# Kernel tuning notes

Measured on AMD Instinct MI355X. Metric: run time of the kernel, lower is better.

## Reference

```python
import jax, jax.numpy as jnp
import numpy as np

N_NODES = 100000
N_EDGES = 3200000
IN_DIM = 128
OUT_DIM = 256  # transform outputs OUT_DIM//2, concat -> OUT_DIM


def setup_inputs() -> dict:
    key = jax.random.key(0)
    ks = jax.random.split(key, 8)
    feats = jax.random.normal(ks[0], (N_NODES, IN_DIM), dtype=jnp.float32)
    src = jax.random.randint(ks[1], (N_EDGES,), 0, N_NODES, dtype=jnp.int64)
    dst = jax.random.randint(ks[2], (N_EDGES,), 0, N_NODES, dtype=jnp.int64)
    # KernelMLP(128, 128, n_hidden=2, scale_hidden=2): 128 -> 256 -> 512 -> 128
    def lin(k, fan_in, fan_out):
        s = 1.0 / np.sqrt(fan_in)
        return jax.random.uniform(k, (fan_in, fan_out), jnp.float32, -s, s)
    W1 = lin(ks[3], 128, 256)
    W2 = lin(ks[4], 256, 512)
    W3 = lin(ks[5], 512, 128)
    b1 = jnp.zeros((256,), jnp.float32)
    b2 = jnp.zeros((512,), jnp.float32)
    b3 = jnp.zeros((128,), jnp.float32)
    return {"features": feats, "src": src, "dst": dst,
            "W1": W1, "b1": b1, "W2": W2, "b2": b2, "W3": W3, "b3": b3}


def kernel_mlp(x, W1, b1, W2, b2, W3, b3):
    # per-node MLP with hidden widths scaling by scale_hidden, ReLU between layers
    h = jax.nn.relu(x @ W1 + b1)
    h = jax.nn.relu(h @ W2 + b2)
    return h @ W3 + b3  # [N, out_dim//2]


def reference(features, src, dst, W1, b1, W2, b2, W3, b3):
    h = kernel_mlp(features, W1, b1, W2, b2, W3, b3)  # [N, 64*2]
    # update_all(copy_src, sum): agg[d] = sum_{(s,d) in E} h[s]
    msgs = h[src]  # [E, out_dim//2] gather (memory bound)
    agg = jax.ops.segment_sum(msgs, dst, num_segments=features.shape[0])
    return jnp.concatenate([h, agg], axis=-1)  # [N, out_dim]
```

## Files before the change

kernel.cpp:

```cpp
#include <hip/hip_runtime.h>
#include <hip/hip_bf16.h>
#include <hip/hip_fp16.h>

typedef __attribute__((ext_vector_type(8))) short short8;
typedef __attribute__((ext_vector_type(4))) short short4v;
typedef __attribute__((ext_vector_type(4))) float f32x4;

#define TM 64
#define SX 136
#define S1 264

#define BK_LG 6
#define BK_N  64
#define MAX_NB 4096
#define PS_CHUNK 16384

__device__ __forceinline__ short f2bf(float x) {
    union { float f; unsigned u; } v; v.f = x;
    unsigned r = v.u + 0x7fffu + ((v.u >> 16) & 1u);
    return (short)(r >> 16);
}

__global__ __launch_bounds__(256) void prep_weights(
        const float* __restrict__ W1, const float* __restrict__ W2,
        const float* __restrict__ W3,
        short* __restrict__ W1t, short* __restrict__ W2t, short* __restrict__ W3t) {
    int i = blockIdx.x * 256 + threadIdx.x;
    if (i < 32768) {
        int n = i >> 7, k = i & 127;
        W1t[i] = f2bf(W1[k * 256 + n]);
    } else if (i < 32768 + 131072) {
        int j = i - 32768;
        int n = j >> 8, k = j & 255;
        W2t[j] = f2bf(W2[k * 512 + n]);
    } else if (i < 229376) {
        int j = i - 163840;
        int n = j >> 9, k = j & 511;
        W3t[j] = f2bf(W3[k * 128 + n]);
    }
}

__global__ __launch_bounds__(512) void mlp_kernel(
        const float* __restrict__ X,
        const float* __restrict__ b1f, const float* __restrict__ b2f,
        const float* __restrict__ b3f,
        const short* __restrict__ W1t, const short* __restrict__ W2t,
        const short* __restrict__ W3t,
        float* __restrict__ out, __half* __restrict__ hh, int n_nodes) {
    __shared__ short lds[TM * S1 + TM * SX];
    short* ldsH1 = lds;
    short* ldsX  = lds + TM * S1;
    short* ldsH2 = ldsX;

    const int tid  = threadIdx.x;
    const int ch   = tid >> 6;
    const int lane = tid & 63;
    const int ln   = lane & 15;
    const int quad = lane >> 4;
    const long node0 = (long)blockIdx.x * TM;

    for (int i = tid; i < TM * 32; i += 512) {
        int r = i >> 5, c4 = i & 31;
        long node = node0 + r;
        float4 v = make_float4(0.f, 0.f, 0.f, 0.f);
        if (node < n_nodes) v = *(const float4*)&X[node * 128 + c4 * 4];
        short4v s;
        s.x = f2bf(v.x); s.y = f2bf(v.y); s.z = f2bf(v.z); s.w = f2bf(v.w);
        *(short4v*)&ldsX[r * SX + c4 * 4] = s;
    }
    __syncthreads();

#pragma unroll
    for (int nt = 0; nt < 2; ++nt) {
        int n = ch * 32 + nt * 16 + ln;
        const short* bp = &W1t[n * 128 + quad * 8];
        short8 b[4];
#pragma unroll
        for (int kk = 0; kk < 4; ++kk) b[kk] = *(const short8*)(bp + kk * 32);
        float bias = b1f[n];
#pragma unroll
        for (int m = 0; m < 4; ++m) {
            f32x4 c = {0.f, 0.f, 0.f, 0.f};
#pragma unroll
            for (int kk = 0; kk < 4; ++kk) {
                short8 a = *(const short8*)&ldsX[(m * 16 + ln) * SX + kk * 32 + quad * 8];
                c = __builtin_amdgcn_mfma_f32_16x16x32_bf16(a, b[kk], c, 0, 0, 0);
            }
#pragma unroll
            for (int rr = 0; rr < 4; ++rr) {
                float h = c[rr] + bias;
                h = h > 0.f ? h : 0.f;
                ldsH1[(m * 16 + quad * 4 + rr) * S1 + n] = f2bf(h);
            }
        }
    }
    __syncthreads();

    f32x4 acc3[4] = {};
#pragma unroll 1
    for (int cc = 0; cc < 4; ++cc) {
        {
            int n2 = cc * 128 + ch * 16 + ln;
            const short* bp = &W2t[n2 * 256 + quad * 8];
            short8 b[8];
#pragma unroll
            for (int kk = 0; kk < 8; ++kk) b[kk] = *(const short8*)(bp + kk * 32);
            float bias = b2f[n2];
            int nl = ch * 16 + ln;
#pragma unroll
            for (int m = 0; m < 4; ++m) {
                f32x4 c = {0.f, 0.f, 0.f, 0.f};
#pragma unroll
                for (int kk = 0; kk < 8; ++kk) {
                    short8 a = *(const short8*)&ldsH1[(m * 16 + ln) * S1 + kk * 32 + quad * 8];
                    c = __builtin_amdgcn_mfma_f32_16x16x32_bf16(a, b[kk], c, 0, 0, 0);
                }
#pragma unroll
                for (int rr = 0; rr < 4; ++rr) {
                    float h = c[rr] + bias;
                    h = h > 0.f ? h : 0.f;
                    ldsH2[(m * 16 + quad * 4 + rr) * SX + nl] = f2bf(h);
                }
            }
        }
        __syncthreads();

        {
            int n3 = ch * 16 + ln;
            const short* bp = &W3t[n3 * 512 + cc * 128 + quad * 8];
            short8 b[4];
#pragma unroll
            for (int kk = 0; kk < 4; ++kk) b[kk] = *(const short8*)(bp + kk * 32);
#pragma unroll
            for (int m = 0; m < 4; ++m) {
#pragma unroll
                for (int kk = 0; kk < 4; ++kk) {
                    short8 a = *(const short8*)&ldsH2[(m * 16 + ln) * SX + kk * 32 + quad * 8];
                    acc3[m] = __builtin_amdgcn_mfma_f32_16x16x32_bf16(a, b[kk], acc3[m], 0, 0, 0);
                }
            }
        }
        __syncthreads();
    }

    {
        int n3 = ch * 16 + ln;
        float bias = b3f[n3];
#pragma unroll
        for (int m = 0; m < 4; ++m) {
#pragma unroll
            for (int rr = 0; rr < 4; ++rr) {
                long node = node0 + m * 16 + quad * 4 + rr;
                if (node < n_nodes) {
                    float v = acc3[m][rr] + bias;
                    out[node * 256 + n3] = v;
                    if (hh) hh[node * 128 + n3] = __float2half(v);
                }
            }
        }
    }
}


__global__ __launch_bounds__(256) void bhist_kernel(
        const int* __restrict__ dst, int* __restrict__ bcnt,
        int n_edges, int nb) {
    __shared__ int h[MAX_NB];
    int tid = threadIdx.x;
    for (int b = tid; b < nb; b += 256) h[b] = 0;
    __syncthreads();
    for (int e = blockIdx.x * 256 + tid; e < n_edges; e += gridDim.x * 256)
        atomicAdd(&h[dst[e] >> BK_LG], 1);
    __syncthreads();
    for (int b = tid; b < nb; b += 256) {
        int c = h[b];
        if (c) atomicAdd(&bcnt[b], c);
    }
}

__global__ __launch_bounds__(256) void bscan_kernel(
        const int* __restrict__ bcnt, int* __restrict__ boffs,
        int* __restrict__ bcur, int nb) {
    __shared__ int s[256];
    int t = threadIdx.x;
    int per = (nb + 255) >> 8;
    int lo = t * per;
    int sum = 0;
    for (int i = 0; i < per; ++i) {
        int b = lo + i;
        if (b < nb) sum += bcnt[b];
    }
    s[t] = sum;
    __syncthreads();
#pragma unroll
    for (int off = 1; off < 256; off <<= 1) {
        int v = (t >= off) ? s[t - off] : 0;
        __syncthreads();
        s[t] += v;
        __syncthreads();
    }
    int base = (t == 0) ? 0 : s[t - 1];
    for (int i = 0; i < per; ++i) {
        int b = lo + i;
        if (b < nb) {
            int c = bcnt[b];
            boffs[b] = base;
            bcur[b]  = base;
            base += c;
        }
    }
    if (t == 255) boffs[nb] = s[255];
}

__global__ __launch_bounds__(256) void bscatter_kernel(
        const int* __restrict__ src, const int* __restrict__ dst,
        int* __restrict__ bcur, unsigned* __restrict__ pairs,
        int n_edges, int nb) {
    __shared__ int h[MAX_NB];
    int tid = threadIdx.x;
    long e0 = (long)blockIdx.x * PS_CHUNK;
    int cnt = n_edges - (int)e0;
    if (cnt > PS_CHUNK) cnt = PS_CHUNK;
    if (cnt <= 0) return;
    for (int b = tid; b < nb; b += 256) h[b] = 0;
    __syncthreads();
    for (int i = tid; i < cnt; i += 256)
        atomicAdd(&h[dst[e0 + i] >> BK_LG], 1);
    __syncthreads();
    for (int b = tid; b < nb; b += 256) {
        int c = h[b];
        h[b] = c ? atomicAdd(&bcur[b], c) : 0;
    }
    __syncthreads();
    for (int i = tid; i < cnt; i += 256) {
        int d = dst[e0 + i];
        int s = src[e0 + i];
        int p = atomicAdd(&h[d >> BK_LG], 1);
        pairs[p] = ((unsigned)(d & (BK_N - 1)) << 26) | (unsigned)s;
    }
}

__global__ __launch_bounds__(256) void bsort_kernel(
        const unsigned* __restrict__ pairs, const int* __restrict__ boffs,
        int* __restrict__ offs, int* __restrict__ esrc,
        int n_nodes, int n_edges) {
    __shared__ int hist[BK_N];
    __shared__ int cur[BK_N];
    const int tid = threadIdx.x;
    const int b = blockIdx.x;
    const int base = boffs[b];
    const int cnt = boffs[b + 1] - base;

    if (tid < BK_N) hist[tid] = 0;
    __syncthreads();
    for (int i = tid; i < cnt; i += 256)
        atomicAdd(&hist[pairs[base + i] >> 26], 1);
    __syncthreads();
    if (tid == 0) {
        int run = base;
#pragma unroll
        for (int k = 0; k < BK_N; ++k) { cur[k] = run; run += hist[k]; }
    }
    __syncthreads();
    if (tid < BK_N) {
        int node = (b << BK_LG) + tid;
        if (node < n_nodes) offs[node] = cur[tid];
    }
    if (b == 0 && tid == 0) offs[n_nodes] = n_edges;
    __syncthreads();
    for (int i = tid; i < cnt; i += 256) {
        unsigned p = pairs[base + i];
        int pos = atomicAdd(&cur[p >> 26], 1);
        esrc[pos] = (int)(p & 0x03FFFFFFu);
    }
}

__global__ __launch_bounds__(256) void agg_half_kernel(
        const int* __restrict__ esrc, const int* __restrict__ offs,
        const __half* __restrict__ hh, float* __restrict__ out, int n_nodes) {
    int node = blockIdx.x * 4 + (threadIdx.x >> 6);
    if (node >= n_nodes) return;
    const int l2 = (threadIdx.x & 63) * 2;
    const int s0 = offs[node];
    const int s1 = offs[node + 1];
    float ax = 0.f, ay = 0.f;
    int j = s0;
    for (; j + 8 <= s1; j += 8) {
        int s[8];
#pragma unroll
        for (int u = 0; u < 8; ++u) s[u] = esrc[j + u];
        __half2 v[8];
#pragma unroll
        for (int u = 0; u < 8; ++u) v[u] = *(const __half2*)&hh[(long)s[u] * 128 + l2];
#pragma unroll
        for (int u = 0; u < 8; ++u) {
            float2 f = __half22float2(v[u]);
            ax += f.x; ay += f.y;
        }
    }
    for (; j < s1; ++j) {
        float2 f = __half22float2(*(const __half2*)&hh[(long)esrc[j] * 128 + l2]);
        ax += f.x; ay += f.y;
    }
    *(float2*)&out[(long)node * 256 + 128 + l2] = make_float2(ax, ay);
}

__global__ __launch_bounds__(256) void agg_kernel(
        const int* __restrict__ esrc, const int* __restrict__ offs,
        float* __restrict__ out, int n_nodes) {
    int node = blockIdx.x * 4 + (threadIdx.x >> 6);
    if (node >= n_nodes) return;
    const int l2 = (threadIdx.x & 63) * 2;
    const int s0 = offs[node];
    const int s1 = offs[node + 1];
    float ax = 0.f, ay = 0.f;
    int j = s0;
    for (; j + 8 <= s1; j += 8) {
        int s[8];
#pragma unroll
        for (int u = 0; u < 8; ++u) s[u] = esrc[j + u];
        float2 v[8];
#pragma unroll
        for (int u = 0; u < 8; ++u) v[u] = *(const float2*)&out[(long)s[u] * 256 + l2];
#pragma unroll
        for (int u = 0; u < 8; ++u) { ax += v[u].x; ay += v[u].y; }
    }
    for (; j < s1; ++j) {
        float2 v = *(const float2*)&out[(long)esrc[j] * 256 + l2];
        ax += v.x; ay += v.y;
    }
    *(float2*)&out[(long)node * 256 + 128 + l2] = make_float2(ax, ay);
}

__global__ __launch_bounds__(256) void bagg_kernel(
        const unsigned* __restrict__ pairs, const int* __restrict__ boffs,
        float* __restrict__ out, int n_nodes) {
    __shared__ float acc[BK_N * 128];
    __shared__ unsigned eb[512];
    const int tid  = threadIdx.x;
    const int col  = tid & 127;
    const int half = tid >> 7;
    const int node0 = blockIdx.x << BK_LG;

    for (int i = tid; i < BK_N * 128; i += 256) acc[i] = 0.f;

    const int s0 = boffs[blockIdx.x];
    const int s1 = boffs[blockIdx.x + 1];

    for (int j0 = s0; j0 < s1; j0 += 512) {
        int m = s1 - j0;
        if (m > 512) m = 512;
        for (int i = tid; i < m; i += 256) eb[i] = pairs[j0 + i];
        __syncthreads();
        int i = half;
        for (; i + 8 <= m; i += 8) {
            unsigned p0 = eb[i], p1 = eb[i + 2], p2 = eb[i + 4], p3 = eb[i + 6];
            float v0 = out[(long)(p0 & 0x03FFFFFFu) * 256 + col];
            float v1 = out[(long)(p1 & 0x03FFFFFFu) * 256 + col];
            float v2 = out[(long)(p2 & 0x03FFFFFFu) * 256 + col];
            float v3 = out[(long)(p3 & 0x03FFFFFFu) * 256 + col];
            atomicAdd(&acc[(p0 >> 26) * 128 + col], v0);
            atomicAdd(&acc[(p1 >> 26) * 128 + col], v1);
            atomicAdd(&acc[(p2 >> 26) * 128 + col], v2);
            atomicAdd(&acc[(p3 >> 26) * 128 + col], v3);
        }
        for (; i < m; i += 2) {
            unsigned pk = eb[i];
            float v = out[(long)(pk & 0x03FFFFFFu) * 256 + col];
            atomicAdd(&acc[(pk >> 26) * 128 + col], v);
        }
        __syncthreads();
    }

    for (int i = tid; i < BK_N * 128; i += 256) {
        int n = node0 + (i >> 7);
        if (n < n_nodes) out[(long)n * 256 + 128 + (i & 127)] = acc[i];
    }
}

__global__ __launch_bounds__(256) void zero_agg(float* __restrict__ out, int n_nodes) {
    int i = blockIdx.x * 256 + threadIdx.x;
    int total = n_nodes * 32;
    for (; i < total; i += gridDim.x * 256) {
        int n = i >> 5, q = i & 31;
        *(float4*)&out[(long)n * 256 + 128 + q * 4] = make_float4(0.f, 0.f, 0.f, 0.f);
    }
}

__global__ __launch_bounds__(256) void edge_agg(
        const int* __restrict__ src, const int* __restrict__ dst,
        float* __restrict__ out, int n_edges) {
    int e = blockIdx.x * 8 + (threadIdx.x >> 5);
    if (e >= n_edges) return;
    int l = threadIdx.x & 31;
    long s = src[e];
    long d = dst[e];
    const float4 v = *(const float4*)&out[s * 256 + l * 4];
    float* p = &out[d * 256 + 128 + l * 4];
    unsafeAtomicAdd(p + 0, v.x);
    unsafeAtomicAdd(p + 1, v.y);
    unsafeAtomicAdd(p + 2, v.z);
    unsafeAtomicAdd(p + 3, v.w);
}

extern "C" void kernel_launch(void* const* d_in, const int* in_sizes, int n_in,
                              void* d_out, int out_size, void* d_ws, size_t ws_size,
                              hipStream_t stream) {
    const float* X   = (const float*)d_in[0];
    const int*   src = (const int*)d_in[1];
    const int*   dst = (const int*)d_in[2];
    const float* W1  = (const float*)d_in[3];
    const float* b1  = (const float*)d_in[4];
    const float* W2  = (const float*)d_in[5];
    const float* b2  = (const float*)d_in[6];
    const float* W3  = (const float*)d_in[7];
    const float* b3  = (const float*)d_in[8];
    float* out = (float*)d_out;

    const int n_nodes = in_sizes[0] / 128;
    const int n_edges = in_sizes[1];
    const int nb = (n_nodes + BK_N - 1) >> BK_LG;

    char* ws = (char*)d_ws;
    short* W1t = (short*)ws;
    short* W2t = W1t + 32768;
    short* W3t = W2t + 131072;

    int* bcnt   = (int*)(ws + 512 * 1024);
    int* boffs  = bcnt + nb;
    int* bcur   = boffs + nb + 1;
    int* offs   = bcur + nb;
    unsigned* pairs = (unsigned*)(offs + n_nodes + 1);
    int* esrc   = (int*)(pairs + n_edges);
    __half* hh  = (__half*)(esrc + n_edges);

    size_t base_need = 512 * 1024 +
                       sizeof(int) * ((size_t)3 * nb + 1 + (size_t)n_nodes + 1);
    size_t need_full = base_need + sizeof(int) * (size_t)2 * n_edges;
    size_t need_half = need_full + (size_t)2 * 128 * n_nodes;
    size_t need_lite = base_need + sizeof(int) * (size_t)n_edges;
    const bool ok_nb = (nb <= MAX_NB) && (n_nodes < (1 << 26)) && (nb >= 1);
    const bool tier_half = ok_nb && ws_size >= need_half;
    const bool tier_full = ok_nb && ws_size >= need_full;
    const bool tier_lite = ok_nb && ws_size >= need_lite;

    prep_weights<<<896, 256, 0, stream>>>(W1, W2, W3, W1t, W2t, W3t);
    mlp_kernel<<<(n_nodes + TM - 1) / TM, 512, 0, stream>>>(
        X, b1, b2, b3, W1t, W2t, W3t, out, tier_half ? hh : (__half*)nullptr,
        n_nodes);

    if (tier_full) {
        hipMemsetAsync(bcnt, 0, (size_t)nb * 4, stream);
        bhist_kernel<<<256, 256, 0, stream>>>(dst, bcnt, n_edges, nb);
        bscan_kernel<<<1, 256, 0, stream>>>(bcnt, boffs, bcur, nb);
        bscatter_kernel<<<(n_edges + PS_CHUNK - 1) / PS_CHUNK, 256, 0, stream>>>(
            src, dst, bcur, pairs, n_edges, nb);
        bsort_kernel<<<nb, 256, 0, stream>>>(pairs, boffs, offs, esrc,
                                             n_nodes, n_edges);
        if (tier_half)
            agg_half_kernel<<<(n_nodes + 3) / 4, 256, 0, stream>>>(
                esrc, offs, hh, out, n_nodes);
        else
            agg_kernel<<<(n_nodes + 3) / 4, 256, 0, stream>>>(
                esrc, offs, out, n_nodes);
    } else if (tier_lite) {
        hipMemsetAsync(bcnt, 0, (size_t)nb * 4, stream);
        bhist_kernel<<<256, 256, 0, stream>>>(dst, bcnt, n_edges, nb);
        bscan_kernel<<<1, 256, 0, stream>>>(bcnt, boffs, bcur, nb);
        bscatter_kernel<<<(n_edges + PS_CHUNK - 1) / PS_CHUNK, 256, 0, stream>>>(
            src, dst, bcur, pairs, n_edges, nb);
        bagg_kernel<<<nb, 256, 0, stream>>>(pairs, boffs, out, n_nodes);
    } else {
        zero_agg<<<3125, 256, 0, stream>>>(out, n_nodes);
        edge_agg<<<(n_edges + 7) / 8, 256, 0, stream>>>(src, dst, out, n_edges);
    }
}
```

Measured before the change: 555.6 us.

## Split fp16 node features into column slabs and aggregate per slab pass

```diff
diff --git a/kernel.cpp b/kernel.cpp
--- a/kernel.cpp
+++ b/kernel.cpp
@@ -5,6 +5,7 @@
 typedef __attribute__((ext_vector_type(8))) short short8;
 typedef __attribute__((ext_vector_type(4))) short short4v;
 typedef __attribute__((ext_vector_type(4))) float f32x4;
+typedef __attribute__((ext_vector_type(2))) float f32x2;
 
 #define TM 64
 #define SX 136
@@ -14,6 +15,7 @@
 #define BK_N  64
 #define MAX_NB 4096
 #define PS_CHUNK 16384
+#define NPASS 8
 
 __device__ __forceinline__ short f2bf(float x) {
     union { float f; unsigned u; } v; v.f = x;
@@ -146,6 +148,7 @@
     {
         int n3 = ch * 16 + ln;
         float bias = b3f[n3];
+        __half* hp = hh ? (hh + (long)ch * n_nodes * 16) : (__half*)nullptr;
 #pragma unroll
         for (int m = 0; m < 4; ++m) {
 #pragma unroll
@@ -154,7 +157,7 @@
                 if (node < n_nodes) {
                     float v = acc3[m][rr] + bias;
                     out[node * 256 + n3] = v;
-                    if (hh) hh[node * 128 + n3] = __float2half(v);
+                    if (hp) hp[node * 16 + ln] = __float2half(v);
                 }
             }
         }
@@ -275,34 +278,52 @@
     }
 }
 
-__global__ __launch_bounds__(256) void agg_half_kernel(
+__global__ __launch_bounds__(256) void agg_split_kernel(
         const int* __restrict__ esrc, const int* __restrict__ offs,
-        const __half* __restrict__ hh, float* __restrict__ out, int n_nodes) {
-    int node = blockIdx.x * 4 + (threadIdx.x >> 6);
+        const __half* __restrict__ hh, float* __restrict__ out,
+        int n_nodes, int nbn) {
+    const int pass = blockIdx.x / nbn;
+    const int nblk = blockIdx.x - pass * nbn;
+    const int node = nblk * 4 + (threadIdx.x >> 6);
     if (node >= n_nodes) return;
-    const int l2 = (threadIdx.x & 63) * 2;
+    const int lane = threadIdx.x & 63;
+    const int slot = lane >> 3;
+    const int c2   = (lane & 7) * 2;
+    const __half* hp = hh + (long)pass * n_nodes * 16;
+
     const int s0 = offs[node];
     const int s1 = offs[node + 1];
     float ax = 0.f, ay = 0.f;
-    int j = s0;
-    for (; j + 8 <= s1; j += 8) {
-        int s[8];
-#pragma unroll
-        for (int u = 0; u < 8; ++u) s[u] = esrc[j + u];
-        __half2 v[8];
-#pragma unroll
-        for (int u = 0; u < 8; ++u) v[u] = *(const __half2*)&hh[(long)s[u] * 128 + l2];
-#pragma unroll
-        for (int u = 0; u < 8; ++u) {
-            float2 f = __half22float2(v[u]);
-            ax += f.x; ay += f.y;
-        }
-    }
-    for (; j < s1; ++j) {
-        float2 f = __half22float2(*(const __half2*)&hh[(long)esrc[j] * 128 + l2]);
+    int j = s0 + slot;
+    for (; j + 24 < s1; j += 32) {
+        int e0 = __builtin_nontemporal_load(&esrc[j]);
+        int e1 = __builtin_nontemporal_load(&esrc[j + 8]);
+        int e2 = __builtin_nontemporal_load(&esrc[j + 16]);
+        int e3 = __builtin_nontemporal_load(&esrc[j + 24]);
+        __half2 v0 = *(const __half2*)&hp[(long)e0 * 16 + c2];
+        __half2 v1 = *(const __half2*)&hp[(long)e1 * 16 + c2];
+        __half2 v2 = *(const __half2*)&hp[(long)e2 * 16 + c2];
+        __half2 v3 = *(const __half2*)&hp[(long)e3 * 16 + c2];
+        float2 f0 = __half22float2(v0), f1 = __half22float2(v1);
+        float2 f2 = __half22float2(v2), f3 = __half22float2(v3);
+        ax += f0.x + f1.x + f2.x + f3.x;
+        ay += f0.y + f1.y + f2.y + f3.y;
+    }
+    for (; j < s1; j += 8) {
+        int e = __builtin_nontemporal_load(&esrc[j]);
+        float2 f = __half22float2(*(const __half2*)&hp[(long)e * 16 + c2]);
         ax += f.x; ay += f.y;
     }
-    *(float2*)&out[(long)node * 256 + 128 + l2] = make_float2(ax, ay);
+#pragma unroll
+    for (int off = 8; off < 64; off <<= 1) {
+        ax += __shfl_xor(ax, off, 64);
+        ay += __shfl_xor(ay, off, 64);
+    }
+    if (lane < 8) {
+        f32x2 r = {ax, ay};
+        __builtin_nontemporal_store(
+            r, (f32x2*)&out[(long)node * 256 + 128 + pass * 16 + lane * 2]);
+    }
 }
 
 __global__ __launch_bounds__(256) void agg_kernel(
@@ -457,12 +478,14 @@
             src, dst, bcur, pairs, n_edges, nb);
         bsort_kernel<<<nb, 256, 0, stream>>>(pairs, boffs, offs, esrc,
                                              n_nodes, n_edges);
-        if (tier_half)
-            agg_half_kernel<<<(n_nodes + 3) / 4, 256, 0, stream>>>(
-                esrc, offs, hh, out, n_nodes);
-        else
+        if (tier_half) {
+            int nbn = (n_nodes + 3) / 4;
+            agg_split_kernel<<<nbn * NPASS, 256, 0, stream>>>(
+                esrc, offs, hh, out, n_nodes, nbn);
+        } else {
             agg_kernel<<<(n_nodes + 3) / 4, 256, 0, stream>>>(
                 esrc, offs, out, n_nodes);
+        }
     } else if (tier_lite) {
         hipMemsetAsync(bcnt, 0, (size_t)nb * 4, stream);
         bhist_kernel<<<256, 256, 0, stream>>>(dst, bcnt, n_edges, nb);
```

Result: slower. 754.9 us (+35.9%).
